# Kernel optimization log

Hardware: AMD Instinct MI355X
Metric: run time of the kernel (lower is better)

## Reference

```python
import jax, jax.numpy as jnp
import numpy as np

# static multi-scale pyramid (must match spatial_shapes array in setup_inputs)
SPATIAL = ((100, 100), (50, 50), (25, 25), (13, 13))
E, H, L, P = 256, 8, 4, 8   # embed_dims, num_heads, num_levels, num_points
BS, NQ = 2, 10000
LEN_VAL = sum(h * w for h, w in SPATIAL)


def _bilinear_gather(val, grid, Hs, Ws):
    """val: [BH, Hs*Ws, d]; grid: [BH, N, 2] in [-1,1].
    Matches F.grid_sample(mode='bilinear', padding_mode='zeros', align_corners=False)."""
    x = (grid[..., 0] + 1.0) * (Ws * 0.5) - 0.5
    y = (grid[..., 1] + 1.0) * (Hs * 0.5) - 0.5
    x0 = jnp.floor(x).astype(jnp.int32)
    y0 = jnp.floor(y).astype(jnp.int32)
    x1, y1 = x0 + 1, y0 + 1
    wx1 = x - x0.astype(x.dtype)
    wy1 = y - y0.astype(y.dtype)
    wx0, wy0 = 1.0 - wx1, 1.0 - wy1

    def corner(xi, yi, w):
        valid = (xi >= 0) & (xi < Ws) & (yi >= 0) & (yi < Hs)
        idx = jnp.clip(yi, 0, Hs - 1) * Ws + jnp.clip(xi, 0, Ws - 1)  # [BH, N]
        v = jnp.take_along_axis(val, idx[..., None], axis=1)          # [BH, N, d]
        return v * (w * valid.astype(w.dtype))[..., None]

    return (corner(x0, y0, wx0 * wy0) + corner(x1, y0, wx1 * wy0)
            + corner(x0, y1, wx0 * wy1) + corner(x1, y1, wx1 * wy1))


def setup_inputs() -> dict:
    key = jax.random.key(0)
    ks = jax.random.split(key, 10)
    scale = 1.0 / np.sqrt(E)
    inp = {
        'query': jax.random.normal(ks[0], (BS, NQ, E), jnp.float32),
        'value': jax.random.normal(ks[1], (BS, LEN_VAL, E), jnp.float32),
        'query_pos': 0.1 * jax.random.normal(ks[2], (BS, NQ, E), jnp.float32),
        'reference_points': jax.random.uniform(ks[3], (BS, NQ, L, 2), jnp.float32),
        'spatial_shapes': jnp.array(SPATIAL, dtype=jnp.int32),
        'W_off': 0.02 * jax.random.normal(ks[4], (E, H * L * P * 2), jnp.float32),
        'b_off': 0.5 * jax.random.normal(ks[5], (H * L * P * 2,), jnp.float32),
        'W_attn': 0.02 * jax.random.normal(ks[6], (E, H * L * P), jnp.float32),
        'b_attn': jnp.zeros((H * L * P,), jnp.float32),
        'W_val': scale * jax.random.normal(ks[7], (E, E), jnp.float32),
        'b_val': jnp.zeros((E,), jnp.float32),
        'W_out': scale * jax.random.normal(ks[8], (E, E), jnp.float32),
        'b_out': jnp.zeros((E,), jnp.float32),
    }
    return inp


def reference(query, value, query_pos, reference_points, spatial_shapes,
              W_off, b_off, W_attn, b_attn, W_val, b_val, W_out, b_out):
    d = E // H
    q = query + query_pos                                        # [bs, nq, E]
    bs, nq, _ = q.shape
    v = (value @ W_val + b_val).reshape(bs, LEN_VAL, H, d)       # [bs, len, H, d]
    off = (q @ W_off + b_off).reshape(bs, nq, H, L, P, 2)
    aw = jax.nn.softmax((q @ W_attn + b_attn).reshape(bs, nq, H, L * P), axis=-1)
    aw = aw.reshape(bs, nq, H, L, P)
    # normalizer is (W, H) per level
    norm = jnp.stack([spatial_shapes[:, 1], spatial_shapes[:, 0]], -1).astype(q.dtype)
    loc = reference_points[:, :, None, :, None, :] + off / norm[None, None, None, :, None, :]
    grids = 2.0 * loc - 1.0                                      # [bs, nq, H, L, P, 2]

    out = jnp.zeros((bs, nq, H, d), q.dtype)
    start = 0
    for lvl, (Hs, Ws) in enumerate(SPATIAL):
        v_l = v[:, start:start + Hs * Ws]                        # [bs, HW, H, d]
        start += Hs * Ws
        v_l = v_l.transpose(0, 2, 1, 3).reshape(bs * H, Hs * Ws, d)
        g_l = grids[:, :, :, lvl].transpose(0, 2, 1, 3, 4).reshape(bs * H, nq * P, 2)
        s = _bilinear_gather(v_l, g_l, Hs, Ws).reshape(bs, H, nq, P, d)
        w_l = aw[:, :, :, lvl].transpose(0, 2, 1, 3)             # [bs, H, nq, P]
        out = out + jnp.einsum('bhnpc,bhnp->bnhc', s, w_l)
    return out.reshape(bs, nq, E) @ W_out + b_out
```

## Files before the change

### kernel.cpp

```cpp
#include <hip/hip_runtime.h>


#define EE   256
#define HH   8
#define LL   4
#define NQq  10000
#define BSB  2
#define LENV 13294
#define MQ   16
#define ROWS_V (BSB * LENV)

#define VWS_OFF 393216

typedef unsigned short u16;
typedef unsigned int   u32;
typedef __attribute__((ext_vector_type(8))) short bf16x8;
typedef __attribute__((ext_vector_type(4))) float f32x4;

__device__ __forceinline__ u32 bf16_of(float f) {
  u32 u = __float_as_uint(f);
  return (u + 0x7FFFu + ((u >> 16) & 1u)) >> 16;
}
__device__ __forceinline__ float blo(u32 u) { return __uint_as_float(u << 16); }
__device__ __forceinline__ float bhi(u32 u) { return __uint_as_float(u & 0xFFFF0000u); }

__device__ __forceinline__ uint4 pack8(const float* f) {
  uint4 u;
  u.x = bf16_of(f[0]) | (bf16_of(f[1]) << 16);
  u.y = bf16_of(f[2]) | (bf16_of(f[3]) << 16);
  u.z = bf16_of(f[4]) | (bf16_of(f[5]) << 16);
  u.w = bf16_of(f[6]) | (bf16_of(f[7]) << 16);
  return u;
}

__device__ __forceinline__ void acc8(float o[8], uint4 q, float w) {
  o[0] += w * blo(q.x); o[1] += w * bhi(q.x);
  o[2] += w * blo(q.y); o[3] += w * bhi(q.y);
  o[4] += w * blo(q.z); o[5] += w * bhi(q.z);
  o[6] += w * blo(q.w); o[7] += w * bhi(q.w);
}

__global__ __launch_bounds__(64) void k_prep(
    const float* __restrict__ W_off, const float* __restrict__ W_attn,
    const float* __restrict__ W_val, const float* __restrict__ W_out,
    u16* __restrict__ wcat, u16* __restrict__ wval, u16* __restrict__ wout) {
  const int tile = blockIdx.x >> 3, s = blockIdx.x & 7;
  const int l = threadIdx.x, quad = l >> 4, r16 = l & 15;
  float f[8];
  u16* dst;
  if (tile < 48) {
    int col = tile * 16 + r16;
#pragma unroll
    for (int j = 0; j < 8; ++j) {
      int k = s * 32 + quad * 8 + j;
      f[j] = (col < 512) ? W_off[k * 512 + col] : W_attn[k * 256 + (col - 512)];
    }
    dst = wcat + ((tile * 8 + s) * 64 + l) * 8;
  } else if (tile < 64) {
    int col = (tile - 48) * 16 + r16;
#pragma unroll
    for (int j = 0; j < 8; ++j) f[j] = W_val[(s * 32 + quad * 8 + j) * 256 + col];
    dst = wval + (((tile - 48) * 8 + s) * 64 + l) * 8;
  } else {
    int col = (tile - 64) * 16 + r16;
#pragma unroll
    for (int j = 0; j < 8; ++j) f[j] = W_out[(s * 32 + quad * 8 + j) * 256 + col];
    dst = wout + (((tile - 64) * 8 + s) * 64 + l) * 8;
  }
  *(uint4*)dst = pack8(f);
}

__global__ __launch_bounds__(512) void k_valproj(
    const float* __restrict__ value, const float* __restrict__ b_val,
    const u16* __restrict__ wval, u16* __restrict__ v_ws) {
  __shared__ __align__(16) u16 sA[64][264];
  const int tid = threadIdx.x;
  const int g0 = blockIdx.x * 64;
#pragma unroll
  for (int ch = 0; ch < 4; ++ch) {
    int fidx = ch * 4096 + tid * 8;
    int row = fidx >> 8, col = fidx & 255;
    int g = g0 + row;
    float fv[8] = {0.f, 0.f, 0.f, 0.f, 0.f, 0.f, 0.f, 0.f};
    if (g < ROWS_V) {
      float4 a = *(const float4*)(value + (long)g * 256 + col);
      float4 b = *(const float4*)(value + (long)g * 256 + col + 4);
      fv[0] = a.x; fv[1] = a.y; fv[2] = a.z; fv[3] = a.w;
      fv[4] = b.x; fv[5] = b.y; fv[6] = b.z; fv[7] = b.w;
    }
    *(uint4*)&sA[row][col] = pack8(fv);
  }
  __syncthreads();
  const int wave = tid >> 6, lane = tid & 63, quad = lane >> 4, r16 = lane & 15;
  f32x4 acc[2][4] = {};
  for (int s = 0; s < 8; ++s) {
    bf16x8 af[4];
#pragma unroll
    for (int mt = 0; mt < 4; ++mt)
      af[mt] = *(const bf16x8*)&sA[mt * 16 + r16][s * 32 + quad * 8];
#pragma unroll
    for (int nt = 0; nt < 2; ++nt) {
      int ntg = wave * 2 + nt;
      bf16x8 bfg = *(const bf16x8*)(wval + ((ntg * 8 + s) * 64 + lane) * 8);
#pragma unroll
      for (int mt = 0; mt < 4; ++mt)
        acc[nt][mt] = __builtin_amdgcn_mfma_f32_16x16x32_bf16(af[mt], bfg, acc[nt][mt], 0, 0, 0);
    }
  }
  __syncthreads();
#pragma unroll
  for (int nt = 0; nt < 2; ++nt) {
    int col = (wave * 2 + nt) * 16 + r16;
    float bias = b_val[col];
#pragma unroll
    for (int mt = 0; mt < 4; ++mt)
#pragma unroll
      for (int rr = 0; rr < 4; ++rr)
        sA[mt * 16 + quad * 4 + rr][col] = (u16)bf16_of(acc[nt][mt][rr] + bias);
  }
  __syncthreads();
#pragma unroll
  for (int it = 0; it < 4; ++it) {
    int chunk = it * 512 + tid;
    int r  = chunk >> 5;
    int hc = chunk & 31;
    int h2 = hc >> 2, qq = hc & 3;
    int g = g0 + r;
    if (g < ROWS_V) {
      int bb = g / LENV, pix = g - bb * LENV;
      *(uint4*)(v_ws + ((long)((bb * 8 + h2) * LENV + pix) * 32 + qq * 8)) =
          *(const uint4*)&sA[r][h2 * 32 + qq * 8];
    }
  }
}

__global__ __launch_bounds__(512, 6) void k_attn(
    const float* __restrict__ query, const float* __restrict__ query_pos,
    const float* __restrict__ refpts,
    const float* __restrict__ b_off, const float* __restrict__ b_attn,
    const float* __restrict__ b_out,
    const u16* __restrict__ wcat, const u16* __restrict__ wout,
    const char* __restrict__ wsb, float* __restrict__ out) {
  __shared__ __align__(16) char smem[49408];
  u16   (*sQ)[264]   = (u16(*)[264])smem;
  float (*sC)[772]   = (float(*)[772])smem;
  uint2 (*sWgt)[256] = (uint2(*)[256])smem;
  u32   (*sOff)[256] = (u32(*)[256])(smem + 32768);
  u16   (*sO)[264]   = (u16(*)[264])smem;

  const int tid = threadIdx.x;
  const int g0 = blockIdx.x * MQ;
  const int b = g0 / NQq;
  const int q0 = g0 - b * NQq;
  const int wave = tid >> 6, lane = tid & 63, quad = lane >> 4, r16 = lane & 15;

  {
    int fidx = tid * 8;
    int row = fidx >> 8, col = fidx & 255;
    long base = ((long)(b * NQq + q0 + row)) * 256 + col;
    float4 a0 = *(const float4*)(query + base);
    float4 a1 = *(const float4*)(query + base + 4);
    float4 p0 = *(const float4*)(query_pos + base);
    float4 p1 = *(const float4*)(query_pos + base + 4);
    float fv[8] = {a0.x + p0.x, a0.y + p0.y, a0.z + p0.z, a0.w + p0.w,
                   a1.x + p1.x, a1.y + p1.y, a1.z + p1.z, a1.w + p1.w};
    *(uint4*)&sQ[row][col] = pack8(fv);
  }
  __syncthreads();

  f32x4 acc[6] = {};
  for (int s = 0; s < 8; ++s) {
    bf16x8 af = *(const bf16x8*)&sQ[r16][s * 32 + quad * 8];
#pragma unroll
    for (int t6 = 0; t6 < 6; ++t6) {
      int tile = wave * 6 + t6;
      bf16x8 bfg = *(const bf16x8*)(wcat + ((tile * 8 + s) * 64 + lane) * 8);
      acc[t6] = __builtin_amdgcn_mfma_f32_16x16x32_bf16(af, bfg, acc[t6], 0, 0, 0);
    }
  }
  __syncthreads();
#pragma unroll
  for (int t6 = 0; t6 < 6; ++t6) {
    int col = (wave * 6 + t6) * 16 + r16;
#pragma unroll
    for (int rr = 0; rr < 4; ++rr)
      sC[quad * 4 + rr][col] = acc[t6][rr];
  }
  __syncthreads();

  uint2 wrecs[8];
  u32   orecs[8];
  {
    const int s = tid & 255, mh = tid >> 8;
    const int l = (s >> 3) & 3;
    const int WlI[4] = {100, 50, 25, 13};
    const int baseI[4] = {0, 10000, 12500, 13125};
    const int Wl = WlI[l], Hl = WlI[l], base = baseI[l];
    const float WlF = (float)Wl;
    const float ba  = b_attn[s];
    const float box = b_off[2 * s], boy = b_off[2 * s + 1];
#pragma unroll
    for (int mm = 0; mm < 8; ++mm) {
      int m = mh * 8 + mm;
      float logit = sC[m][512 + s] + ba;
      float mx = logit;
      mx = fmaxf(mx, __shfl_xor(mx, 1));
      mx = fmaxf(mx, __shfl_xor(mx, 2));
      mx = fmaxf(mx, __shfl_xor(mx, 4));
      mx = fmaxf(mx, __shfl_xor(mx, 8));
      mx = fmaxf(mx, __shfl_xor(mx, 16));
      float e = __expf(logit - mx);
      float sum = e;
      sum += __shfl_xor(sum, 1);
      sum += __shfl_xor(sum, 2);
      sum += __shfl_xor(sum, 4);
      sum += __shfl_xor(sum, 8);
      sum += __shfl_xor(sum, 16);
      float w = e * __frcp_rn(sum);
      float ax = sC[m][2 * s], ay = sC[m][2 * s + 1];
      float2 rp = *(const float2*)(refpts + (((long)(b * NQq + q0 + m)) * LL + l) * 2);
      float x = rp.x * WlF + (ax + box) - 0.5f;
      float y = rp.y * WlF + (ay + boy) - 0.5f;
      float fx0 = floorf(x), fy0 = floorf(y);
      int x0 = (int)fx0, y0 = (int)fy0;
      float fx = x - fx0, fy = y - fy0;
      bool xv0 = (x0 >= 0) & (x0 < Wl);
      bool xv1 = (x0 >= -1) & (x0 < Wl - 1);
      bool yv0 = (y0 >= 0) & (y0 < Hl);
      bool yv1 = (y0 >= -1) & (y0 < Hl - 1);
      float w00 = w * (1.f - fx) * (1.f - fy) * (float)(xv0 & yv0);
      float w01 = w * fx * (1.f - fy) * (float)(xv1 & yv0);
      float w10 = w * (1.f - fx) * fy * (float)(xv0 & yv1);
      float w11 = w * fx * fy * (float)(xv1 & yv1);
      int x0a = min(max(x0, -1), Wl - 1);
      int y0a = min(max(y0, -1), Hl - 1);
      int y1c = min(max(y0 + 1, 0), Hl - 1);
      int o00u = base + y0a * Wl + x0a;
      u32 dyu  = (u32)((y1c - y0a) * Wl);
      wrecs[mm].x = bf16_of(w00) | (bf16_of(w01) << 16);
      wrecs[mm].y = bf16_of(w10) | (bf16_of(w11) << 16);
      orecs[mm]   = (u32)(o00u + 128) | (dyu << 14);
    }
  }
  __syncthreads();
  {
    const int s = tid & 255, mh = tid >> 8;
    const int jsw = (s & 224) | ((s + (s >> 5)) & 31);
#pragma unroll
    for (int mm = 0; mm < 8; ++mm) {
      sWgt[mh * 8 + mm][jsw] = wrecs[mm];
      sOff[mh * 8 + mm][jsw] = orecs[mm];
    }
  }
  __syncthreads();

  {
    const int c4 = tid & 3, hh = (tid >> 2) & 7, m = tid >> 5;
    const u32 vbm = (u32)VWS_OFF + (u32)(b * 8 + hh) * (u32)(LENV * 64)
                  + (u32)c4 * 16u - 8192u;
    float oacc[8] = {};
#pragma unroll 8
    for (int i = 0; i < 32; ++i) {
      const int srow = (hh << 5) | ((i + hh) & 31);
      uint2 wr = sWgt[m][srow];
      u32   po = sOff[m][srow];
      u32 off0 = vbm + ((po & 0x3FFFu) << 6);
      u32 off1 = off0 + ((po >> 14) << 6);
      uint4 q00 = *(const uint4*)(wsb + off0);
      uint4 q01 = *(const uint4*)(wsb + off0 + 64);
      uint4 q10 = *(const uint4*)(wsb + off1);
      uint4 q11 = *(const uint4*)(wsb + off1 + 64);
      float w00 = blo(wr.x), w01 = bhi(wr.x);
      float w10 = blo(wr.y), w11 = bhi(wr.y);
      acc8(oacc, q00, w00);
      acc8(oacc, q01, w01);
      acc8(oacc, q10, w10);
      acc8(oacc, q11, w11);
    }
    __syncthreads();
    *(uint4*)&sO[m][hh * 32 + c4 * 8] = pack8(oacc);
  }
  __syncthreads();

  f32x4 acc2[2] = {};
  for (int s = 0; s < 8; ++s) {
    bf16x8 af = *(const bf16x8*)&sO[r16][s * 32 + quad * 8];
#pragma unroll
    for (int t2 = 0; t2 < 2; ++t2) {
      int tile = wave * 2 + t2;
      bf16x8 bfg = *(const bf16x8*)(wout + ((tile * 8 + s) * 64 + lane) * 8);
      acc2[t2] = __builtin_amdgcn_mfma_f32_16x16x32_bf16(af, bfg, acc2[t2], 0, 0, 0);
    }
  }
#pragma unroll
  for (int t2 = 0; t2 < 2; ++t2) {
    int col = (wave * 2 + t2) * 16 + r16;
    float bias = b_out[col];
#pragma unroll
    for (int rr = 0; rr < 4; ++rr) {
      int row = quad * 4 + rr;
      out[((long)(b * NQq + q0 + row)) * 256 + col] = acc2[t2][rr] + bias;
    }
  }
}

extern "C" void kernel_launch(void* const* d_in, const int* in_sizes, int n_in,
                              void* d_out, int out_size, void* d_ws, size_t ws_size,
                              hipStream_t stream) {
  const float* query     = (const float*)d_in[0];
  const float* value     = (const float*)d_in[1];
  const float* query_pos = (const float*)d_in[2];
  const float* refpts    = (const float*)d_in[3];
  const float* W_off     = (const float*)d_in[5];
  const float* b_off     = (const float*)d_in[6];
  const float* W_attn    = (const float*)d_in[7];
  const float* b_attn    = (const float*)d_in[8];
  const float* W_val     = (const float*)d_in[9];
  const float* b_val     = (const float*)d_in[10];
  const float* W_out     = (const float*)d_in[11];
  const float* b_out     = (const float*)d_in[12];
  float* out = (float*)d_out;

  char* ws = (char*)d_ws;
  u16* wcat = (u16*)ws;
  u16* v_ws = (u16*)(ws + VWS_OFF);
  u16* wval = (u16*)(ws + VWS_OFF + 13613056);
  u16* wout = (u16*)(ws + VWS_OFF + 13613056 + 131072);

  k_prep<<<dim3(80 * 8), dim3(64), 0, stream>>>(W_off, W_attn, W_val, W_out,
                                                wcat, wval, wout);
  k_valproj<<<dim3((ROWS_V + 63) / 64), dim3(512), 0, stream>>>(value, b_val, wval, v_ws);
  k_attn<<<dim3(BSB * NQq / MQ), dim3(512), 0, stream>>>(
      query, query_pos, refpts, b_off, b_attn, b_out, wcat, wout, ws, out);
}
```

Baseline: 236.8 us.

## Split query projection into a separate 64-row MFMA kernel writing bf16 offsets and logits

After: 250.5 us. 1.06x slower.

```diff
diff --git a/kernel.cpp b/kernel.cpp
--- a/kernel.cpp
+++ b/kernel.cpp
@@ -9,8 +9,10 @@
 #define LENV 13294
 #define MQ   16
 #define ROWS_V (BSB * LENV)
+#define NROWS (BSB * NQq)
 
 #define VWS_OFF 393216
+#define GC_OFF  14268416
 
 typedef unsigned short u16;
 typedef unsigned int   u32;
@@ -23,6 +25,7 @@
 }
 __device__ __forceinline__ float blo(u32 u) { return __uint_as_float(u << 16); }
 __device__ __forceinline__ float bhi(u32 u) { return __uint_as_float(u & 0xFFFF0000u); }
+__device__ __forceinline__ float b2f(u32 u) { return __uint_as_float(u << 16); }
 
 __device__ __forceinline__ uint4 pack8(const float* f) {
   uint4 u;
@@ -50,10 +53,11 @@
   u16* dst;
   if (tile < 48) {
     int col = tile * 16 + r16;
+    int sc = col / 3, kp = col - sc * 3;
 #pragma unroll
     for (int j = 0; j < 8; ++j) {
-      int k = s * 32 + quad * 8 + j;
-      f[j] = (col < 512) ? W_off[k * 512 + col] : W_attn[k * 256 + (col - 512)];
+      int kk = s * 32 + quad * 8 + j;
+      f[j] = (kp < 2) ? W_off[kk * 512 + 2 * sc + kp] : W_attn[kk * 256 + sc];
     }
     dst = wcat + ((tile * 8 + s) * 64 + l) * 8;
   } else if (tile < 64) {
@@ -134,62 +138,87 @@
   }
 }
 
-__global__ __launch_bounds__(512, 6) void k_attn(
+__global__ __launch_bounds__(512) void k_qproj(
     const float* __restrict__ query, const float* __restrict__ query_pos,
+    const u16* __restrict__ wcat, u16* __restrict__ gC) {
+  __shared__ __align__(16) u16 sA[64][264];
+  const int tid = threadIdx.x;
+  const int g0 = blockIdx.x * 64;
+#pragma unroll
+  for (int ch = 0; ch < 4; ++ch) {
+    int fidx = ch * 4096 + tid * 8;
+    int row = fidx >> 8, col = fidx & 255;
+    int g = g0 + row;
+    float fv[8] = {0.f, 0.f, 0.f, 0.f, 0.f, 0.f, 0.f, 0.f};
+    if (g < NROWS) {
+      long base = (long)g * 256 + col;
+      float4 a0 = *(const float4*)(query + base);
+      float4 a1 = *(const float4*)(query + base + 4);
+      float4 p0 = *(const float4*)(query_pos + base);
+      float4 p1 = *(const float4*)(query_pos + base + 4);
+      fv[0] = a0.x + p0.x; fv[1] = a0.y + p0.y; fv[2] = a0.z + p0.z; fv[3] = a0.w + p0.w;
+      fv[4] = a1.x + p1.x; fv[5] = a1.y + p1.y; fv[6] = a1.z + p1.z; fv[7] = a1.w + p1.w;
+    }
+    *(uint4*)&sA[row][col] = pack8(fv);
+  }
+  __syncthreads();
+  const int wave = tid >> 6, lane = tid & 63, quad = lane >> 4, r16 = lane & 15;
+  f32x4 acc[6][4] = {};
+  for (int s = 0; s < 8; ++s) {
+    bf16x8 af[4];
+#pragma unroll
+    for (int mt = 0; mt < 4; ++mt)
+      af[mt] = *(const bf16x8*)&sA[mt * 16 + r16][s * 32 + quad * 8];
+#pragma unroll
+    for (int t6 = 0; t6 < 6; ++t6) {
+      int tile = wave * 6 + t6;
+      bf16x8 bfg = *(const bf16x8*)(wcat + ((tile * 8 + s) * 64 + lane) * 8);
+#pragma unroll
+      for (int mt = 0; mt < 4; ++mt)
+        acc[t6][mt] = __builtin_amdgcn_mfma_f32_16x16x32_bf16(af[mt], bfg, acc[t6][mt], 0, 0, 0);
+    }
+  }
+#pragma unroll
+  for (int t6 = 0; t6 < 6; ++t6) {
+    int col = (wave * 6 + t6) * 16 + r16;
+#pragma unroll
+    for (int mt = 0; mt < 4; ++mt)
+#pragma unroll
+      for (int rr = 0; rr < 4; ++rr) {
+        int g = g0 + mt * 16 + quad * 4 + rr;
+        if (g < NROWS) gC[(long)g * 768 + col] = (u16)bf16_of(acc[t6][mt][rr]);
+      }
+  }
+}
+
+__global__ __launch_bounds__(512, 8) void k_attn(
     const float* __restrict__ refpts,
     const float* __restrict__ b_off, const float* __restrict__ b_attn,
     const float* __restrict__ b_out,
-    const u16* __restrict__ wcat, const u16* __restrict__ wout,
+    const u16* __restrict__ gC, const u16* __restrict__ wout,
     const char* __restrict__ wsb, float* __restrict__ out) {
-  __shared__ __align__(16) char smem[49408];
-  u16   (*sQ)[264]   = (u16(*)[264])smem;
-  float (*sC)[772]   = (float(*)[772])smem;
+  __shared__ __align__(16) char smem[40960];
+  u16*  sG           = (u16*)smem;
   uint2 (*sWgt)[256] = (uint2(*)[256])smem;
-  u32   (*sOff)[256] = (u32(*)[256])(smem + 32768);
+  u16   (*sOff)[256] = (u16(*)[256])(smem + 32768);
   u16   (*sO)[264]   = (u16(*)[264])smem;
 
   const int tid = threadIdx.x;
   const int g0 = blockIdx.x * MQ;
   const int b = g0 / NQq;
-  const int q0 = g0 - b * NQq;
   const int wave = tid >> 6, lane = tid & 63, quad = lane >> 4, r16 = lane & 15;
 
   {
-    int fidx = tid * 8;
-    int row = fidx >> 8, col = fidx & 255;
-    long base = ((long)(b * NQq + q0 + row)) * 256 + col;
-    float4 a0 = *(const float4*)(query + base);
-    float4 a1 = *(const float4*)(query + base + 4);
-    float4 p0 = *(const float4*)(query_pos + base);
-    float4 p1 = *(const float4*)(query_pos + base + 4);
-    float fv[8] = {a0.x + p0.x, a0.y + p0.y, a0.z + p0.z, a0.w + p0.w,
-                   a1.x + p1.x, a1.y + p1.y, a1.z + p1.z, a1.w + p1.w};
-    *(uint4*)&sQ[row][col] = pack8(fv);
-  }
-  __syncthreads();
-
-  f32x4 acc[6] = {};
-  for (int s = 0; s < 8; ++s) {
-    bf16x8 af = *(const bf16x8*)&sQ[r16][s * 32 + quad * 8];
-#pragma unroll
-    for (int t6 = 0; t6 < 6; ++t6) {
-      int tile = wave * 6 + t6;
-      bf16x8 bfg = *(const bf16x8*)(wcat + ((tile * 8 + s) * 64 + lane) * 8);
-      acc[t6] = __builtin_amdgcn_mfma_f32_16x16x32_bf16(af, bfg, acc[t6], 0, 0, 0);
-    }
-  }
-  __syncthreads();
-#pragma unroll
-  for (int t6 = 0; t6 < 6; ++t6) {
-    int col = (wave * 6 + t6) * 16 + r16;
-#pragma unroll
-    for (int rr = 0; rr < 4; ++rr)
-      sC[quad * 4 + rr][col] = acc[t6][rr];
+    int row = tid >> 5, col = (tid & 31) * 24;
+    const u16* src = gC + (long)(g0 + row) * 768 + col;
+    u16* dst = sG + row * 768 + col;
+    *(uint4*)(dst)      = *(const uint4*)(src);
+    *(uint4*)(dst + 8)  = *(const uint4*)(src + 8);
+    *(uint4*)(dst + 16) = *(const uint4*)(src + 16);
   }
   __syncthreads();
 
   uint2 wrecs[8];
-  u32   orecs[8];
   {
     const int s = tid & 255, mh = tid >> 8;
     const int l = (s >> 3) & 3;
@@ -199,10 +228,13 @@
     const float WlF = (float)Wl;
     const float ba  = b_attn[s];
     const float box = b_off[2 * s], boy = b_off[2 * s + 1];
+    const int jsw = (s & 224) | ((s + (s >> 5)) & 31);
 #pragma unroll
     for (int mm = 0; mm < 8; ++mm) {
       int m = mh * 8 + mm;
-      float logit = sC[m][512 + s] + ba;
+      const u16* cp = sG + m * 768 + 3 * s;
+      float ax = b2f(cp[0]), ay = b2f(cp[1]);
+      float logit = b2f(cp[2]) + ba;
       float mx = logit;
       mx = fmaxf(mx, __shfl_xor(mx, 1));
       mx = fmaxf(mx, __shfl_xor(mx, 2));
@@ -216,9 +248,8 @@
       sum += __shfl_xor(sum, 4);
       sum += __shfl_xor(sum, 8);
       sum += __shfl_xor(sum, 16);
-      float w = e * __frcp_rn(sum);
-      float ax = sC[m][2 * s], ay = sC[m][2 * s + 1];
-      float2 rp = *(const float2*)(refpts + (((long)(b * NQq + q0 + m)) * LL + l) * 2);
+      float w = e / sum;
+      float2 rp = *(const float2*)(refpts + (((long)(g0 + m)) * LL + l) * 2);
       float x = rp.x * WlF + (ax + box) - 0.5f;
       float y = rp.y * WlF + (ay + boy) - 0.5f;
       float fx0 = floorf(x), fy0 = floorf(y);
@@ -236,10 +267,10 @@
       int y0a = min(max(y0, -1), Hl - 1);
       int y1c = min(max(y0 + 1, 0), Hl - 1);
       int o00u = base + y0a * Wl + x0a;
-      u32 dyu  = (u32)((y1c - y0a) * Wl);
+      int dyf  = y1c - y0a;
       wrecs[mm].x = bf16_of(w00) | (bf16_of(w01) << 16);
       wrecs[mm].y = bf16_of(w10) | (bf16_of(w11) << 16);
-      orecs[mm]   = (u32)(o00u + 128) | (dyu << 14);
+      sOff[m][jsw] = (u16)((o00u + 128) | (dyf << 14));
     }
   }
   __syncthreads();
@@ -247,10 +278,7 @@
     const int s = tid & 255, mh = tid >> 8;
     const int jsw = (s & 224) | ((s + (s >> 5)) & 31);
 #pragma unroll
-    for (int mm = 0; mm < 8; ++mm) {
-      sWgt[mh * 8 + mm][jsw] = wrecs[mm];
-      sOff[mh * 8 + mm][jsw] = orecs[mm];
-    }
+    for (int mm = 0; mm < 8; ++mm) sWgt[mh * 8 + mm][jsw] = wrecs[mm];
   }
   __syncthreads();
 
@@ -259,23 +287,27 @@
     const u32 vbm = (u32)VWS_OFF + (u32)(b * 8 + hh) * (u32)(LENV * 64)
                   + (u32)c4 * 16u - 8192u;
     float oacc[8] = {};
-#pragma unroll 8
-    for (int i = 0; i < 32; ++i) {
-      const int srow = (hh << 5) | ((i + hh) & 31);
-      uint2 wr = sWgt[m][srow];
-      u32   po = sOff[m][srow];
-      u32 off0 = vbm + ((po & 0x3FFFu) << 6);
-      u32 off1 = off0 + ((po >> 14) << 6);
-      uint4 q00 = *(const uint4*)(wsb + off0);
-      uint4 q01 = *(const uint4*)(wsb + off0 + 64);
-      uint4 q10 = *(const uint4*)(wsb + off1);
-      uint4 q11 = *(const uint4*)(wsb + off1 + 64);
-      float w00 = blo(wr.x), w01 = bhi(wr.x);
-      float w10 = blo(wr.y), w11 = bhi(wr.y);
-      acc8(oacc, q00, w00);
-      acc8(oacc, q01, w01);
-      acc8(oacc, q10, w10);
-      acc8(oacc, q11, w11);
+    const u32 wl64tab[4] = {6400u, 3200u, 1600u, 832u};
+#pragma unroll
+    for (int lv = 0; lv < 4; ++lv) {
+      const u32 wl64 = wl64tab[lv];
+#pragma unroll 4
+      for (int ii = 0; ii < 8; ++ii) {
+        const int i = lv * 8 + ii;
+        const int srow = (hh << 5) | ((i + hh) & 31);
+        uint2 wr = sWgt[m][srow];
+        u32   po = (u32)sOff[m][srow];
+        u32 off0 = vbm + ((po & 0x3FFFu) << 6);
+        u32 off1 = off0 + (po >> 14) * wl64;
+        uint4 q00 = *(const uint4*)(wsb + off0);
+        uint4 q01 = *(const uint4*)(wsb + off0 + 64);
+        uint4 q10 = *(const uint4*)(wsb + off1);
+        uint4 q11 = *(const uint4*)(wsb + off1 + 64);
+        acc8(oacc, q00, blo(wr.x));
+        acc8(oacc, q01, bhi(wr.x));
+        acc8(oacc, q10, blo(wr.y));
+        acc8(oacc, q11, bhi(wr.y));
+      }
     }
     __syncthreads();
     *(uint4*)&sO[m][hh * 32 + c4 * 8] = pack8(oacc);
@@ -299,7 +331,7 @@
 #pragma unroll
     for (int rr = 0; rr < 4; ++rr) {
       int row = quad * 4 + rr;
-      out[((long)(b * NQq + q0 + row)) * 256 + col] = acc2[t2][rr] + bias;
+      out[((long)(g0 + row)) * 256 + col] = acc2[t2][rr] + bias;
     }
   }
 }
@@ -326,10 +358,12 @@
   u16* v_ws = (u16*)(ws + VWS_OFF);
   u16* wval = (u16*)(ws + VWS_OFF + 13613056);
   u16* wout = (u16*)(ws + VWS_OFF + 13613056 + 131072);
+  u16* gC   = (u16*)(ws + GC_OFF);
 
   k_prep<<<dim3(80 * 8), dim3(64), 0, stream>>>(W_off, W_attn, W_val, W_out,
                                                 wcat, wval, wout);
+  k_qproj<<<dim3((NROWS + 63) / 64), dim3(512), 0, stream>>>(query, query_pos, wcat, gC);
   k_valproj<<<dim3((ROWS_V + 63) / 64), dim3(512), 0, stream>>>(value, b_val, wval, v_ws);
   k_attn<<<dim3(BSB * NQq / MQ), dim3(512), 0, stream>>>(
-      query, query_pos, refpts, b_off, b_attn, b_out, wcat, wout, ws, out);
-}
+      refpts, b_off, b_attn, b_out, gC, wout, ws, out);
+}
```

## Store projected values pixel-major, interleave offset/attn columns, shrink LDS for occupancy

Applied to the files above, without the earlier changes.

New measurement: 236.1 us. Within noise of the previous version (-0.3%).

```diff
diff --git a/kernel.cpp b/kernel.cpp
--- a/kernel.cpp
+++ b/kernel.cpp
@@ -23,6 +23,7 @@
 }
 __device__ __forceinline__ float blo(u32 u) { return __uint_as_float(u << 16); }
 __device__ __forceinline__ float bhi(u32 u) { return __uint_as_float(u & 0xFFFF0000u); }
+__device__ __forceinline__ float b2f(u32 u) { return __uint_as_float(u << 16); }
 
 __device__ __forceinline__ uint4 pack8(const float* f) {
   uint4 u;
@@ -50,10 +51,11 @@
   u16* dst;
   if (tile < 48) {
     int col = tile * 16 + r16;
+    int sc = col / 3, kp = col - sc * 3;
 #pragma unroll
     for (int j = 0; j < 8; ++j) {
-      int k = s * 32 + quad * 8 + j;
-      f[j] = (col < 512) ? W_off[k * 512 + col] : W_attn[k * 256 + (col - 512)];
+      int kk = s * 32 + quad * 8 + j;
+      f[j] = (kp < 2) ? W_off[kk * 512 + 2 * sc + kp] : W_attn[kk * 256 + sc];
     }
     dst = wcat + ((tile * 8 + s) * 64 + l) * 8;
   } else if (tile < 64) {
@@ -123,41 +125,36 @@
   for (int it = 0; it < 4; ++it) {
     int chunk = it * 512 + tid;
     int r  = chunk >> 5;
-    int hc = chunk & 31;
-    int h2 = hc >> 2, qq = hc & 3;
+    int cc = (chunk & 31) * 8;
     int g = g0 + r;
-    if (g < ROWS_V) {
-      int bb = g / LENV, pix = g - bb * LENV;
-      *(uint4*)(v_ws + ((long)((bb * 8 + h2) * LENV + pix) * 32 + qq * 8)) =
-          *(const uint4*)&sA[r][h2 * 32 + qq * 8];
-    }
-  }
-}
-
-__global__ __launch_bounds__(512, 6) void k_attn(
+    if (g < ROWS_V)
+      *(uint4*)(v_ws + (long)g * 256 + cc) = *(const uint4*)&sA[r][cc];
+  }
+}
+
+__global__ __launch_bounds__(512, 8) void k_attn(
     const float* __restrict__ query, const float* __restrict__ query_pos,
     const float* __restrict__ refpts,
     const float* __restrict__ b_off, const float* __restrict__ b_attn,
     const float* __restrict__ b_out,
     const u16* __restrict__ wcat, const u16* __restrict__ wout,
     const char* __restrict__ wsb, float* __restrict__ out) {
-  __shared__ __align__(16) char smem[49408];
+  __shared__ __align__(16) char smem[40960];
   u16   (*sQ)[264]   = (u16(*)[264])smem;
-  float (*sC)[772]   = (float(*)[772])smem;
+  u16   (*sC)[772]   = (u16(*)[772])smem;
   uint2 (*sWgt)[256] = (uint2(*)[256])smem;
-  u32   (*sOff)[256] = (u32(*)[256])(smem + 32768);
+  u16   (*sOff)[256] = (u16(*)[256])(smem + 32768);
   u16   (*sO)[264]   = (u16(*)[264])smem;
 
   const int tid = threadIdx.x;
   const int g0 = blockIdx.x * MQ;
   const int b = g0 / NQq;
-  const int q0 = g0 - b * NQq;
   const int wave = tid >> 6, lane = tid & 63, quad = lane >> 4, r16 = lane & 15;
 
   {
     int fidx = tid * 8;
     int row = fidx >> 8, col = fidx & 255;
-    long base = ((long)(b * NQq + q0 + row)) * 256 + col;
+    long base = ((long)(g0 + row)) * 256 + col;
     float4 a0 = *(const float4*)(query + base);
     float4 a1 = *(const float4*)(query + base + 4);
     float4 p0 = *(const float4*)(query_pos + base);
@@ -184,12 +181,11 @@
     int col = (wave * 6 + t6) * 16 + r16;
 #pragma unroll
     for (int rr = 0; rr < 4; ++rr)
-      sC[quad * 4 + rr][col] = acc[t6][rr];
+      sC[quad * 4 + rr][col] = (u16)bf16_of(acc[t6][rr]);
   }
   __syncthreads();
 
   uint2 wrecs[8];
-  u32   orecs[8];
   {
     const int s = tid & 255, mh = tid >> 8;
     const int l = (s >> 3) & 3;
@@ -199,10 +195,13 @@
     const float WlF = (float)Wl;
     const float ba  = b_attn[s];
     const float box = b_off[2 * s], boy = b_off[2 * s + 1];
+    const int jsw = (s & 224) | ((s + (s >> 5)) & 31);
 #pragma unroll
     for (int mm = 0; mm < 8; ++mm) {
       int m = mh * 8 + mm;
-      float logit = sC[m][512 + s] + ba;
+      const u16* cp = &sC[m][3 * s];
+      float ax = b2f(cp[0]), ay = b2f(cp[1]);
+      float logit = b2f(cp[2]) + ba;
       float mx = logit;
       mx = fmaxf(mx, __shfl_xor(mx, 1));
       mx = fmaxf(mx, __shfl_xor(mx, 2));
@@ -216,9 +215,8 @@
       sum += __shfl_xor(sum, 4);
       sum += __shfl_xor(sum, 8);
       sum += __shfl_xor(sum, 16);
-      float w = e * __frcp_rn(sum);
-      float ax = sC[m][2 * s], ay = sC[m][2 * s + 1];
-      float2 rp = *(const float2*)(refpts + (((long)(b * NQq + q0 + m)) * LL + l) * 2);
+      float w = e / sum;
+      float2 rp = *(const float2*)(refpts + (((long)(g0 + m)) * LL + l) * 2);
       float x = rp.x * WlF + (ax + box) - 0.5f;
       float y = rp.y * WlF + (ay + boy) - 0.5f;
       float fx0 = floorf(x), fy0 = floorf(y);
@@ -235,11 +233,11 @@
       int x0a = min(max(x0, -1), Wl - 1);
       int y0a = min(max(y0, -1), Hl - 1);
       int y1c = min(max(y0 + 1, 0), Hl - 1);
-      int o00u = base + y0a * Wl + x0a;
-      u32 dyu  = (u32)((y1c - y0a) * Wl);
+      int p00 = base + y0a * Wl + x0a;
+      int dyf = y1c - y0a;
       wrecs[mm].x = bf16_of(w00) | (bf16_of(w01) << 16);
       wrecs[mm].y = bf16_of(w10) | (bf16_of(w11) << 16);
-      orecs[mm]   = (u32)(o00u + 128) | (dyu << 14);
+      sOff[m][jsw] = (u16)((p00 + 128) | (dyf << 14));
     }
   }
   __syncthreads();
@@ -247,35 +245,36 @@
     const int s = tid & 255, mh = tid >> 8;
     const int jsw = (s & 224) | ((s + (s >> 5)) & 31);
 #pragma unroll
-    for (int mm = 0; mm < 8; ++mm) {
-      sWgt[mh * 8 + mm][jsw] = wrecs[mm];
-      sOff[mh * 8 + mm][jsw] = orecs[mm];
-    }
+    for (int mm = 0; mm < 8; ++mm) sWgt[mh * 8 + mm][jsw] = wrecs[mm];
   }
   __syncthreads();
 
   {
     const int c4 = tid & 3, hh = (tid >> 2) & 7, m = tid >> 5;
-    const u32 vbm = (u32)VWS_OFF + (u32)(b * 8 + hh) * (u32)(LENV * 64)
-                  + (u32)c4 * 16u - 8192u;
+    const u32 vbm = (u32)VWS_OFF + (u32)(b * LENV) * 512u + (u32)hh * 64u
+                  + (u32)c4 * 16u - 65536u;
     float oacc[8] = {};
-#pragma unroll 8
-    for (int i = 0; i < 32; ++i) {
-      const int srow = (hh << 5) | ((i + hh) & 31);
-      uint2 wr = sWgt[m][srow];
-      u32   po = sOff[m][srow];
-      u32 off0 = vbm + ((po & 0x3FFFu) << 6);
-      u32 off1 = off0 + ((po >> 14) << 6);
-      uint4 q00 = *(const uint4*)(wsb + off0);
-      uint4 q01 = *(const uint4*)(wsb + off0 + 64);
-      uint4 q10 = *(const uint4*)(wsb + off1);
-      uint4 q11 = *(const uint4*)(wsb + off1 + 64);
-      float w00 = blo(wr.x), w01 = bhi(wr.x);
-      float w10 = blo(wr.y), w11 = bhi(wr.y);
-      acc8(oacc, q00, w00);
-      acc8(oacc, q01, w01);
-      acc8(oacc, q10, w10);
-      acc8(oacc, q11, w11);
+    const u32 wltab[4] = {51200u, 25600u, 12800u, 6656u};
+#pragma unroll
+    for (int lv = 0; lv < 4; ++lv) {
+      const u32 wl = wltab[lv];
+#pragma unroll 4
+      for (int ii = 0; ii < 8; ++ii) {
+        const int i = lv * 8 + ii;
+        const int srow = (hh << 5) | ((i + hh) & 31);
+        uint2 wr = sWgt[m][srow];
+        u32   po = (u32)sOff[m][srow];
+        u32 off0 = vbm + ((po & 0x3FFFu) << 9);
+        u32 off1 = off0 + (po >> 14) * wl;
+        uint4 q00 = *(const uint4*)(wsb + off0);
+        uint4 q01 = *(const uint4*)(wsb + off0 + 512);
+        uint4 q10 = *(const uint4*)(wsb + off1);
+        uint4 q11 = *(const uint4*)(wsb + off1 + 512);
+        acc8(oacc, q00, blo(wr.x));
+        acc8(oacc, q01, bhi(wr.x));
+        acc8(oacc, q10, blo(wr.y));
+        acc8(oacc, q11, bhi(wr.y));
+      }
     }
     __syncthreads();
     *(uint4*)&sO[m][hh * 32 + c4 * 8] = pack8(oacc);
@@ -299,7 +298,7 @@
 #pragma unroll
     for (int rr = 0; rr < 4; ++rr) {
       int row = quad * 4 + rr;
-      out[((long)(b * NQq + q0 + row)) * 256 + col] = acc2[t2][rr] + bias;
+      out[((long)(g0 + row)) * 256 + col] = acc2[t2][rr] + bias;
     }
   }
 }
```
